# Performance work log

Hardware: AMD Instinct MI355X
Metric: run time of the kernel (lower is better)

The kernel has to match this reference:

```python
import jax, jax.numpy as jnp
import numpy as np

H = 100          # hidden_size
D = 2 * H        # mod / q_enc feature dim (BiDAF hidden)
B, L, G, Q = 16, 2048, 12, 64
NEG = -1e30


def _bidaf(c, q, c_mask, q_mask, cw, qw, cqw, bias):
    """BiDAF attention. c:(B,Lc,D) q:(B,Q,D) -> (B,Lc,4D). Eval mode (no dropout)."""
    s0 = c @ cw                                    # (B,Lc,1)
    s1 = jnp.swapaxes(q @ qw, 1, 2)                # (B,1,Q)
    s2 = jnp.einsum('bld,bqd->blq', c * cqw, q)    # (B,Lc,Q)
    s = s0 + s1 + s2 + bias
    p_q = jax.nn.softmax(jnp.where(q_mask[:, None, :] > 0, s, NEG), axis=2)  # c2q
    p_c = jax.nn.softmax(jnp.where(c_mask[:, :, None] > 0, s, NEG), axis=1)  # q2c
    a = p_q @ q                                    # (B,Lc,D)
    qc = jnp.einsum('blq,bld->bqd', p_c, c)        # s2^T @ c, reassociated
    b2 = p_q @ qc                                  # == (p_q @ p_c^T) @ c
    return jnp.concatenate([c, a, c * a, c * b2], axis=-1)


def setup_inputs() -> dict:
    ks = jax.random.split(jax.random.key(0), 16)
    f32 = jnp.float32
    inp = {
        'att': jax.random.normal(ks[0], (B, L, 8 * H), f32),
        'mod': jax.random.normal(ks[1], (B, L, D), f32),
        'gap_indices': jax.random.randint(ks[2], (B, G), 0, L),
        'mask': jnp.ones((B, L), jnp.int32),
        'q_enc': jax.random.normal(ks[3], (B, Q, D), f32),
        'q_mask': jnp.ones((B, Q), jnp.int32),
        'c_weight': jax.random.normal(ks[4], (D, 1), f32) * 0.07,
        'q_weight': jax.random.normal(ks[5], (D, 1), f32) * 0.07,
        'cq_weight': jax.random.normal(ks[6], (1, 1, D), f32) * 0.07,
        'bidaf_bias': jnp.zeros((1,), f32),
        'w_att': jax.random.normal(ks[7], (3 * 8 * H, 1), f32) * 0.02,
        'b_att': jnp.zeros((1,), f32),
        'w_mod': jax.random.normal(ks[8], (3 * 2 * H, 1), f32) * 0.04,
        'b_mod': jnp.zeros((1,), f32),
        'w_att2': jax.random.normal(ks[9], (3 * 8 * H, 1), f32) * 0.02,
        'b_att2': jnp.zeros((1,), f32),
        'w_att_s': jax.random.normal(ks[10], (3 * 8 * H, 1), f32) * 0.02,
        'b_att_s': jnp.zeros((1,), f32),
        'w_mod_s': jax.random.normal(ks[11], (3 * 2 * H, 1), f32) * 0.04,
        'b_mod_s': jnp.zeros((1,), f32),
        'w_att_s2': jax.random.normal(ks[12], (3 * 8 * H, 1), f32) * 0.02,
        'b_att_s2': jnp.zeros((1,), f32),
    }
    return inp


def reference(att, mod, gap_indices, mask, q_enc, q_mask,
              c_weight, q_weight, cq_weight, bidaf_bias,
              w_att, b_att, w_mod, b_mod, w_att2, b_att2,
              w_att_s, b_att_s, w_mod_s, b_mod_s, w_att_s2, b_att_s2):
    Bz, Lz, _ = mod.shape
    idx_b = jnp.arange(Bz)[:, None]
    att_gaps = att[idx_b, gap_indices]            # (B,G,8H)
    mod_gaps = mod[idx_b, gap_indices]            # (B,G,2H)
    att2_gaps = _bidaf(mod_gaps, q_enc, jnp.ones_like(gap_indices), q_mask,
                       c_weight, q_weight, cq_weight, bidaf_bias)  # (B,G,8H)

    maskf = mask.astype(jnp.float32)
    cnt0 = maskf.sum(1)[:, None]                  # (B,1)
    pool0_mod = jnp.concatenate([mod.max(1), mod.sum(1) / cnt0], -1)   # (B,4H)
    pool0_att = jnp.concatenate([att.max(1), att.sum(1) / cnt0], -1)   # (B,16H)
    pool0_att2 = jnp.zeros((Bz, 2 * 8 * H), mod.dtype)                 # (B,1600)

    positions = jnp.arange(Lz)[None, :]           # (1,L)

    def step(carry, gid):                          # gid: (B,)
        wm = (positions >= gid[:, None] - 12) & (positions <= gid[:, None] + 12) & (mask > 0)
        wmf = wm.astype(jnp.float32)
        cnt = wmf.sum(1)[:, None]                  # (B,1)
        modw = mod * wmf[:, :, None]
        attw = att * wmf[:, :, None]
        pm = jnp.concatenate([modw.max(1), modw.sum(1) / cnt], -1)
        pa = jnp.concatenate([attw.max(1), attw.sum(1) / cnt], -1)
        a2 = _bidaf(modw, q_enc, wm.astype(jnp.int32), q_mask,
                    c_weight, q_weight, cq_weight, bidaf_bias)   # (B,L,8H)
        p2 = jnp.concatenate([a2.max(1), a2.sum(1) / cnt], -1)
        return carry, (pm, pa, p2)

    _, (pm, pa, p2) = jax.lax.scan(step, None, gap_indices[:, 1:].T)
    pools_mod = jnp.concatenate([pool0_mod[:, None], jnp.swapaxes(pm, 0, 1)], 1)   # (B,G,4H)
    pools_att = jnp.concatenate([pool0_att[:, None], jnp.swapaxes(pa, 0, 1)], 1)   # (B,G,16H)
    pools_att2 = jnp.concatenate([pool0_att2[:, None], jnp.swapaxes(p2, 0, 1)], 1) # (B,G,16H)

    mod_cat = jnp.concatenate([mod_gaps, pools_mod], -1)      # (B,G,6H)
    att_cat = jnp.concatenate([att_gaps, pools_att], -1)      # (B,G,24H)
    att2_cat = jnp.concatenate([att2_gaps, pools_att2], -1)   # (B,G,24H)

    logit_start = (att_cat[:, :1] @ w_att_s + b_att_s
                   + mod_cat[:, :1] @ w_mod_s + b_mod_s
                   + att2_cat[:, :1] @ w_att_s2 + b_att_s2)
    logit_rest = (att_cat[:, 1:] @ w_att + b_att
                  + mod_cat[:, 1:] @ w_mod + b_mod
                  + att2_cat[:, 1:] @ w_att2 + b_att2)
    logits = jnp.concatenate([logit_start, logit_rest], 1)[:, :, 0]   # (B,G)
    return logits
```

## Files before the change

kernel.cpp:

```cpp
#include <hip/hip_runtime.h>
#include <math.h>


constexpr int LL = 2048;
constexpr int GG = 12;
constexpr int QQ = 64;
constexpr int DD = 200;
constexpr int AD = 800;
constexpr int NW = 25;
constexpr float FNEG = -1e30f;

constexpr size_t OFF_QET  = 0;
constexpr size_t OFF_S1   = 204800;
constexpr size_t OFF_PART = 205824;
constexpr size_t OFF_PAM  = 205840;
constexpr size_t OFF_PAS  = 410640;
constexpr size_t OFF_PMM  = 615440;
constexpr size_t OFF_PMS  = 666640;

__device__ __forceinline__ float dot4(const float4 a, const float4 b) {
  return a.x*b.x + a.y*b.y + a.z*b.z + a.w*b.w;
}
__device__ __forceinline__ float4 max4(const float4 a, const float4 b) {
  return make_float4(fmaxf(a.x,b.x), fmaxf(a.y,b.y), fmaxf(a.z,b.z), fmaxf(a.w,b.w));
}
__device__ __forceinline__ float4 add4(const float4 a, const float4 b) {
  return make_float4(a.x+b.x, a.y+b.y, a.z+b.z, a.w+b.w);
}
__device__ __forceinline__ float wave_sum(float v) {
  #pragma unroll
  for (int o = 32; o > 0; o >>= 1) v += __shfl_down(v, o, 64);
  return v;
}

__global__ __launch_bounds__(256) void k_pre(const float* __restrict__ q_enc,
                                             const float* __restrict__ qwv,
                                             const float* __restrict__ cqw,
                                             float* __restrict__ ws) {
  const int qs = blockIdx.x, b = blockIdx.y, t = threadIdx.x;
  const int ql = t >> 4, jt = t & 15;
  const int q = qs * 16 + ql;
  float s1 = 0.f;
  #pragma unroll
  for (int k = 0; k < 4; ++k) {
    const int j = jt + 16 * k;
    if (j < 50) {
      const float4 v  = ((const float4*)(q_enc + ((size_t)b * QQ + q) * DD))[j];
      const float4 cw = ((const float4*)cqw)[j];
      const float4 qw = ((const float4*)qwv)[j];
      float4 o; o.x = v.x*cw.x; o.y = v.y*cw.y; o.z = v.z*cw.z; o.w = v.w*cw.w;
      ((float4*)(ws + OFF_QET + (size_t)b * 12800))[j * 64 + q] = o;
      s1 += dot4(v, qw);
    }
  }
  s1 += __shfl_xor(s1, 1, 64);
  s1 += __shfl_xor(s1, 2, 64);
  s1 += __shfl_xor(s1, 4, 64);
  s1 += __shfl_xor(s1, 8, 64);
  if (jt == 0) ws[OFF_S1 + b * QQ + q] = s1;
}

__global__ __launch_bounds__(1024) void k_pool_att(const float* __restrict__ att,
                                                   float* __restrict__ ws) {
  const int ch = blockIdx.x, b = blockIdx.y, t = threadIdx.x;
  __shared__ __align__(16) float stA[4][200][8];
  if (t < 800) {
    const int qt = t / 200, col = t - qt * 200;
    const float4* p = (const float4*)(att + ((size_t)b * LL + ch * 128 + qt * 32) * AD) + col;
    float4 m = make_float4(-3e38f, -3e38f, -3e38f, -3e38f);
    float4 s = make_float4(0.f, 0.f, 0.f, 0.f);
    for (int i = 0; i < 32; i += 4) {
      const float4 v0 = p[(size_t)(i + 0) * 200];
      const float4 v1 = p[(size_t)(i + 1) * 200];
      const float4 v2 = p[(size_t)(i + 2) * 200];
      const float4 v3 = p[(size_t)(i + 3) * 200];
      m = max4(m, max4(max4(v0, v1), max4(v2, v3)));
      s = add4(s, add4(add4(v0, v1), add4(v2, v3)));
    }
    *(float4*)&stA[qt][col][0] = m;
    *(float4*)&stA[qt][col][4] = s;
  }
  __syncthreads();
  if (t < 200) {
    float4 m = *(const float4*)&stA[0][t][0];
    float4 s = *(const float4*)&stA[0][t][4];
    #pragma unroll
    for (int qt = 1; qt < 4; ++qt) {
      m = max4(m, *(const float4*)&stA[qt][t][0]);
      s = add4(s, *(const float4*)&stA[qt][t][4]);
    }
    ((float4*)(ws + OFF_PAM))[(size_t)(b * 16 + ch) * 200 + t] = m;
    ((float4*)(ws + OFF_PAS))[(size_t)(b * 16 + ch) * 200 + t] = s;
  }
}

__global__ __launch_bounds__(512) void k_pool_mod(const float* __restrict__ mod,
                                                  float* __restrict__ ws) {
  const int ch = blockIdx.x, b = blockIdx.y, t = threadIdx.x;
  __shared__ __align__(16) float stM[8][50][8];
  if (t < 400) {
    const int rg = t / 50, col = t - rg * 50;
    const float4* p = (const float4*)(mod + ((size_t)b * LL + ch * 128 + rg * 16) * DD) + col;
    float4 m = make_float4(-3e38f, -3e38f, -3e38f, -3e38f);
    float4 s = make_float4(0.f, 0.f, 0.f, 0.f);
    for (int i = 0; i < 16; i += 4) {
      const float4 v0 = p[(size_t)(i + 0) * 50];
      const float4 v1 = p[(size_t)(i + 1) * 50];
      const float4 v2 = p[(size_t)(i + 2) * 50];
      const float4 v3 = p[(size_t)(i + 3) * 50];
      m = max4(m, max4(max4(v0, v1), max4(v2, v3)));
      s = add4(s, add4(add4(v0, v1), add4(v2, v3)));
    }
    *(float4*)&stM[rg][col][0] = m;
    *(float4*)&stM[rg][col][4] = s;
  }
  __syncthreads();
  if (t < 50) {
    float4 m = *(const float4*)&stM[0][t][0];
    float4 s = *(const float4*)&stM[0][t][4];
    #pragma unroll
    for (int rg = 1; rg < 8; ++rg) {
      m = max4(m, *(const float4*)&stM[rg][t][0]);
      s = add4(s, *(const float4*)&stM[rg][t][4]);
    }
    ((float4*)(ws + OFF_PMM))[(size_t)(b * 16 + ch) * 50 + t] = m;
    ((float4*)(ws + OFF_PMS))[(size_t)(b * 16 + ch) * 50 + t] = s;
  }
}

__global__ __launch_bounds__(1024, 4) void k_main(
    const float* __restrict__ att, const float* __restrict__ mod,
    const int* __restrict__ gaps, const int* __restrict__ mask,
    const float* __restrict__ q_enc, const int* __restrict__ q_mask,
    const float* __restrict__ cwv,
    const float* __restrict__ wA,  const float* __restrict__ bA,
    const float* __restrict__ wM,  const float* __restrict__ bM,
    const float* __restrict__ wA2, const float* __restrict__ bA2,
    const float* __restrict__ wAs, const float* __restrict__ wMs,
    const float* __restrict__ wA2s,
    float* __restrict__ ws, float* __restrict__ out) {

  const int x = blockIdx.x, b = blockIdx.y, t = threadIdx.x;
  const int w = t >> 6, lane = t & 63;

  __shared__ __align__(16) float cA[37][200];
  __shared__ __align__(16) float sA[37][68];
  __shared__ __align__(16) float pqS[27][68];
  __shared__ __align__(16) float pqT[64][28];
  __shared__ __align__(16) float MTS[25][28];
  __shared__ float MgS[12];
  __shared__ float statS[4][2600];
  __shared__ float s0A[37];
  __shared__ float s1S[64];
  __shared__ float red[16];
  __shared__ int rowsS[37];
  __shared__ int qmS[64];
  __shared__ int cntS, gidS;

  if (t >= 64 && t < 80) ((int4*)qmS)[t - 64] = ((const int4*)(q_mask + b * QQ))[t - 64];
  if (w == 15) {
    const int gid = gaps[b * GG + x];
    if (lane == 0) gidS = gid;
    if (lane >= 32 && lane < 44) rowsS[NW + lane - 32] = gaps[b * GG + (lane - 32)];
    bool ok = false; int pos = 0;
    if (x > 0 && lane < NW) {
      const int lo = max(gid - 12, 0), hi = min(gid + 12, LL - 1);
      pos = lo + lane;
      ok = (pos <= hi) && (mask[(size_t)b * LL + pos] > 0);
    }
    const unsigned long long bal = __ballot(ok);
    if (lane < NW) rowsS[lane] = gid;
    if (ok) rowsS[__popcll(bal & ((1ull << lane) - 1ull))] = pos;
    if (lane == 0) cntS = (x > 0) ? (int)__popcll(bal) : 0;
  }
  __syncthreads();

  for (int i = t; i < 37 * 50; i += 1024) {
    const int rr = i / 50, dc = (i - rr * 50) * 4;
    *(float4*)&cA[rr][dc] = *(const float4*)(mod + ((size_t)b * LL + rowsS[rr]) * DD + dc);
  }
  if (t >= 896 && t < 960) s1S[t - 896] = ws[OFF_S1 + b * QQ + (t - 896)];
  __syncthreads();

  if (t < 37) {
    float a = 0.f;
    for (int k = 0; k < 50; ++k)
      a += dot4(*(const float4*)&cA[t][k * 4], ((const float4*)cwv)[k]);
    s0A[t] = a;
  }
  {
    const int rBase = (x == 0) ? NW : 0;
    const int nR = (x == 0) ? GG : 37;
    const float* qet = ws + OFF_QET + (size_t)b * 12800;
    const int r0 = w, r1 = w + 16, r2r = w + 32;
    const bool h0 = r0 < nR, h1 = r1 < nR, h2 = r2r < nR;
    const int rr0 = rBase + (h0 ? r0 : 0);
    const int rr1 = rBase + (h1 ? r1 : 0);
    const int rr2 = rBase + (h2 ? r2r : 0);
    float a0 = 0.f, a1 = 0.f, a2 = 0.f;
    for (int j = 0; j < 50; ++j) {
      const float4 qv = ((const float4*)qet)[j * 64 + lane];
      a0 += dot4(*(const float4*)&cA[rr0][j * 4], qv);
      a1 += dot4(*(const float4*)&cA[rr1][j * 4], qv);
      a2 += dot4(*(const float4*)&cA[rr2][j * 4], qv);
    }
    if (h0) sA[rr0][lane] = a0;
    if (h1) sA[rr1][lane] = a1;
    if (h2) sA[rr2][lane] = a2;
  }
  __syncthreads();

  float pv[8];
  const bool rowAct = (t < 216);
  const int grp = t >> 3, j8 = t & 7;
  if (rowAct) {
    if (grp < NW && grp >= cntS) {
      #pragma unroll
      for (int k = 0; k < 8; ++k) pv[k] = 0.f;
    } else {
      const int srow = (grp < NW) ? grp : (NW + x);
      #pragma unroll
      for (int k = 0; k < 8; ++k) {
        const int q = j8 * 8 + k;
        const float s = (grp == 26) ? s1S[q] : (sA[srow][q] + s1S[q]);
        pv[k] = (qmS[q] > 0) ? s : FNEG;
      }
      float m = pv[0];
      #pragma unroll
      for (int k = 1; k < 8; ++k) m = fmaxf(m, pv[k]);
      m = fmaxf(m, __shfl_xor(m, 1, 64));
      m = fmaxf(m, __shfl_xor(m, 2, 64));
      m = fmaxf(m, __shfl_xor(m, 4, 64));
      float sum = 0.f;
      #pragma unroll
      for (int k = 0; k < 8; ++k) { pv[k] = expf(pv[k] - m); sum += pv[k]; }
      sum += __shfl_xor(sum, 1, 64);
      sum += __shfl_xor(sum, 2, 64);
      sum += __shfl_xor(sum, 4, 64);
      const float inv = 1.f / sum;
      #pragma unroll
      for (int k = 0; k < 8; ++k) pv[k] *= inv;
    }
  }
  float pcv[37];
  const bool colAct = (t >= 256 && t < 320);
  if (colAct) {
    const int qc = t - 256;
    const int cnt = cntS;
    float mW = -3e38f;
    for (int r = 0; r < NW; ++r)
      if (r < cnt) mW = fmaxf(mW, sA[r][qc] + s0A[r]);
    float sum = 0.f;
    for (int r = 0; r < NW; ++r) {
      float e = 0.f;
      if (r < cnt) { e = expf(sA[r][qc] + s0A[r] - mW); sum += e; }
      pcv[r] = e;
    }
    const float inv = (cnt > 0) ? (1.f / sum) : 0.f;
    for (int r = 0; r < NW; ++r) pcv[r] *= inv;
    float mG = -3e38f;
    for (int g = 0; g < GG; ++g) mG = fmaxf(mG, sA[NW + g][qc] + s0A[NW + g]);
    sum = 0.f;
    for (int g = 0; g < GG; ++g) {
      const float e = expf(sA[NW + g][qc] + s0A[NW + g] - mG);
      pcv[NW + g] = e; sum += e;
    }
    const float invg = 1.f / sum;
    for (int g = 0; g < GG; ++g) pcv[NW + g] *= invg;
  }
  __syncthreads();

  if (rowAct) {
    *(float4*)&pqS[grp][j8 * 8]     = make_float4(pv[0], pv[1], pv[2], pv[3]);
    *(float4*)&pqS[grp][j8 * 8 + 4] = make_float4(pv[4], pv[5], pv[6], pv[7]);
    #pragma unroll
    for (int k = 0; k < 8; ++k) pqT[j8 * 8 + k][grp] = pv[k];
  }
  if (colAct) {
    const int qc = t - 256;
    for (int r = 0; r < 37; ++r) sA[r][qc] = pcv[r];
  }
  if (t >= 320 && t < 384) pqT[t - 320][27] = 0.f;
  __syncthreads();

  if (t < 637) {
    int pr, pc;
    if (t < 625) { pr = t / 25; pc = t - pr * 25; }
    else         { pr = 25;     pc = NW + (t - 625); }
    float s = 0.f;
    #pragma unroll 4
    for (int k4 = 0; k4 < 16; ++k4)
      s += dot4(*(const float4*)&pqS[pr][k4 * 4], *(const float4*)&sA[pc][k4 * 4]);
    if (t < 625) MTS[pc][pr] = s; else MgS[t - 625] = s;
  }
  if (t >= 640 && t < 715) { const int e = t - 640; MTS[e / 3][25 + e % 3] = 0.f; }
  __syncthreads();

  {
    const int slab = t >> 8, d = t & 255;
    if (d < 200) {
      const int r0 = 8 * slab;
      float a[8] = {0,0,0,0,0,0,0,0};
      float bb[8] = {0,0,0,0,0,0,0,0};
      const float* qe = q_enc + (size_t)b * QQ * DD + d;
      if (slab < 3) {
        #pragma unroll 4
        for (int q = 0; q < QQ; ++q) {
          const float vq = qe[(size_t)q * DD];
          const float4 p0 = *(const float4*)&pqT[q][r0];
          const float4 p1 = *(const float4*)&pqT[q][r0 + 4];
          a[0] += p0.x*vq; a[1] += p0.y*vq; a[2] += p0.z*vq; a[3] += p0.w*vq;
          a[4] += p1.x*vq; a[5] += p1.y*vq; a[6] += p1.z*vq; a[7] += p1.w*vq;
        }
        #pragma unroll 5
        for (int r2 = 0; r2 < NW; ++r2) {
          const float cv = cA[r2][d];
          const float4 m0 = *(const float4*)&MTS[r2][r0];
          const float4 m1 = *(const float4*)&MTS[r2][r0 + 4];
          bb[0] += m0.x*cv; bb[1] += m0.y*cv; bb[2] += m0.z*cv; bb[3] += m0.w*cv;
          bb[4] += m1.x*cv; bb[5] += m1.y*cv; bb[6] += m1.z*cv; bb[7] += m1.w*cv;
        }
      } else {
        #pragma unroll 4
        for (int q = 0; q < QQ; ++q) {
          const float vq = qe[(size_t)q * DD];
          const float4 p0 = *(const float4*)&pqT[q][24];
          a[0] += p0.x*vq; a[1] += p0.y*vq; a[2] += p0.z*vq; a[3] += p0.w*vq;
        }
        #pragma unroll 5
        for (int r2 = 0; r2 < NW; ++r2) {
          const float cv = cA[r2][d];
          const float4 m0 = *(const float4*)&MTS[r2][24];
          bb[0] += m0.x*cv;
        }
      }
      const int cnt = cntS;
      float mxa = -3e38f, sma = 0.f, mxca = -3e38f, smca = 0.f;
      float mxcb = -3e38f, smcb = 0.f, aG = 0.f;
      if (slab < 3) {
        #pragma unroll
        for (int k = 0; k < 8; ++k) {
          const int r = r0 + k;
          if (r < cnt) {
            const float av = a[k], cv = cA[r][d];
            mxa = fmaxf(mxa, av); sma += av;
            const float ca = cv * av; mxca = fmaxf(mxca, ca); smca += ca;
            const float cb = cv * bb[k]; mxcb = fmaxf(mxcb, cb); smcb += cb;
          }
        }
      } else {
        if (24 < cnt) {
          const float av = a[0], cv = cA[24][d];
          mxa = fmaxf(mxa, av); sma += av;
          const float ca = cv * av; mxca = fmaxf(mxca, ca); smca += ca;
          const float cb = cv * bb[0]; mxcb = fmaxf(mxcb, cb); smcb += cb;
        }
        aG = a[1];
        const float ac = a[2];
        mxa = fmaxf(mxa, ac);
        sma += (float)(LL - cnt) * ac;
      }
      float* sp = &statS[slab][d * 13];
      sp[0] = mxa; sp[1] = sma; sp[2] = mxca; sp[3] = smca;
      sp[4] = mxcb; sp[5] = smcb; sp[6] = aG;
    }
  }
  __syncthreads();

  float acc = 0.f;
  const float* wa  = x ? wA  : wAs;
  const float* wm  = x ? wM  : wMs;
  const float* wa2 = x ? wA2 : wA2s;
  if (t < 200) {
    const int d = t;
    float mxa = -3e38f, sma = 0.f, mxca = 0.f, smca = 0.f, mxcb = 0.f, smcb = 0.f;
    #pragma unroll
    for (int s = 0; s < 4; ++s) {
      const float* sp = &statS[s][d * 13];
      mxa = fmaxf(mxa, sp[0]); sma += sp[1];
      mxca = fmaxf(mxca, sp[2]); smca += sp[3];
      mxcb = fmaxf(mxcb, sp[4]); smcb += sp[5];
    }
    const float aG = statS[3][d * 13 + 6];
    const float cg = cA[NW + x][d];
    float b2G = 0.f;
    #pragma unroll
    for (int g = 0; g < GG; ++g) b2G += MgS[g] * cA[NW + g][d];
    acc += cg * (wa2[d] + wm[d]) + aG * wa2[DD + d]
         + cg * aG * wa2[2 * DD + d] + cg * b2G * wa2[3 * DD + d];
    if (x > 0) {
      const int cnt = cntS;
      const float invc = 1.f / (float)cnt;
      float mxc = 0.f, smc = 0.f;
      #pragma unroll
      for (int r = 0; r < NW; ++r) {
        if (r < cnt) { const float cv = cA[r][d]; mxc = fmaxf(mxc, cv); smc += cv; }
      }
      acc += mxc * (wm[DD + d] + wa2[AD + d]) + smc * invc * (wm[2 * DD + d] + wa2[2 * AD + d]);
      acc += mxa * wa2[AD + DD + d]       + sma  * invc * wa2[2 * AD + DD + d];
      acc += mxca * wa2[AD + 2 * DD + d]  + smca * invc * wa2[2 * AD + 2 * DD + d];
      acc += mxcb * wa2[AD + 3 * DD + d]  + smcb * invc * wa2[2 * AD + 3 * DD + d];
    }
    const float4 w0 = ((const float4*)wa)[t];
    const float4 ar = ((const float4*)(att + ((size_t)b * LL + gidS) * AD))[t];
    acc += dot4(ar, w0);
    if (x > 0) {
      const float4 w1 = ((const float4*)(wa + AD))[t];
      const float4 w2 = ((const float4*)(wa + 2 * AD))[t];
      float4 mx = make_float4(0.f, 0.f, 0.f, 0.f);
      float4 sm = make_float4(0.f, 0.f, 0.f, 0.f);
      const int cnt = cntS;
      for (int r = 0; r < NW; ++r) {
        if (r < cnt) {
          const float4 v = ((const float4*)(att + ((size_t)b * LL + rowsS[r]) * AD))[t];
          mx = max4(mx, v); sm = add4(sm, v);
        }
      }
      const float invc = 1.f / (float)cnt;
      acc += dot4(mx, w1) + invc * dot4(sm, w2);
    }
  }
  const float wsum = wave_sum(acc);
  if (lane == 0) red[w] = wsum;
  __syncthreads();
  if (t == 0) {
    float s = 0.f;
    #pragma unroll
    for (int i = 0; i < 16; ++i) s += red[i];
    if (x == 0) ws[OFF_PART + b] = s;
    else out[b * GG + x] = s + bA[0] + bM[0] + bA2[0];
  }
}

__global__ __launch_bounds__(256) void k_finish(const int* __restrict__ mask,
    const float* __restrict__ wAs, const float* __restrict__ bAs,
    const float* __restrict__ wMs, const float* __restrict__ bMs,
    const float* __restrict__ bA2s,
    const float* __restrict__ ws, float* __restrict__ out) {
  const int b = blockIdx.x, t = threadIdx.x;
  __shared__ float red[4];
  __shared__ float inv0S;
  int cm = 0;
  for (int l = t; l < LL; l += 256) cm += (mask[(size_t)b * LL + l] > 0) ? 1 : 0;
  const float cf = wave_sum((float)cm);
  if ((t & 63) == 0) red[t >> 6] = cf;
  __syncthreads();
  if (t == 0) inv0S = 1.f / (red[0] + red[1] + red[2] + red[3]);
  __syncthreads();
  const float inv0 = inv0S;
  float acc = 0.f;
  if (t < 200) {
    float4 m = ((const float4*)(ws + OFF_PAM))[(size_t)(b * 16) * 200 + t];
    float4 s = ((const float4*)(ws + OFF_PAS))[(size_t)(b * 16) * 200 + t];
    for (int ch = 1; ch < 16; ++ch) {
      m = max4(m, ((const float4*)(ws + OFF_PAM))[(size_t)(b * 16 + ch) * 200 + t]);
      s = add4(s, ((const float4*)(ws + OFF_PAS))[(size_t)(b * 16 + ch) * 200 + t]);
    }
    acc += dot4(m, ((const float4*)(wAs + AD))[t]) + inv0 * dot4(s, ((const float4*)(wAs + 2 * AD))[t]);
  }
  if (t < 50) {
    float4 m = ((const float4*)(ws + OFF_PMM))[(size_t)(b * 16) * 50 + t];
    float4 s = ((const float4*)(ws + OFF_PMS))[(size_t)(b * 16) * 50 + t];
    for (int ch = 1; ch < 16; ++ch) {
      m = max4(m, ((const float4*)(ws + OFF_PMM))[(size_t)(b * 16 + ch) * 50 + t]);
      s = add4(s, ((const float4*)(ws + OFF_PMS))[(size_t)(b * 16 + ch) * 50 + t]);
    }
    acc += dot4(m, ((const float4*)(wMs + DD))[t]) + inv0 * dot4(s, ((const float4*)(wMs + 2 * DD))[t]);
  }
  __syncthreads();
  const float tot = wave_sum(acc);
  if ((t & 63) == 0) red[t >> 6] = tot;
  __syncthreads();
  if (t == 0)
    out[b * GG] = red[0] + red[1] + red[2] + red[3] + ws[OFF_PART + b]
                + bAs[0] + bMs[0] + bA2s[0];
}

extern "C" void kernel_launch(void* const* d_in, const int* in_sizes, int n_in,
                              void* d_out, int out_size, void* d_ws, size_t ws_size,
                              hipStream_t stream) {
  (void)in_sizes; (void)n_in; (void)out_size; (void)ws_size;
  const float* att    = (const float*)d_in[0];
  const float* mod    = (const float*)d_in[1];
  const int*   gaps   = (const int*)  d_in[2];
  const int*   mask   = (const int*)  d_in[3];
  const float* q_enc  = (const float*)d_in[4];
  const int*   q_mask = (const int*)  d_in[5];
  const float* cwv    = (const float*)d_in[6];
  const float* qwv    = (const float*)d_in[7];
  const float* cqw    = (const float*)d_in[8];
  const float* wA     = (const float*)d_in[10];
  const float* bA     = (const float*)d_in[11];
  const float* wM     = (const float*)d_in[12];
  const float* bM     = (const float*)d_in[13];
  const float* wA2    = (const float*)d_in[14];
  const float* bA2    = (const float*)d_in[15];
  const float* wAs    = (const float*)d_in[16];
  const float* bAs    = (const float*)d_in[17];
  const float* wMs    = (const float*)d_in[18];
  const float* bMs    = (const float*)d_in[19];
  const float* wA2s   = (const float*)d_in[20];
  const float* bA2s   = (const float*)d_in[21];
  float* out = (float*)d_out;
  float* ws  = (float*)d_ws;

  hipLaunchKernelGGL(k_pre, dim3(4, 16), dim3(256), 0, stream, q_enc, qwv, cqw, ws);
  hipLaunchKernelGGL(k_main, dim3(GG, 16), dim3(1024), 0, stream,
                     att, mod, gaps, mask, q_enc, q_mask, cwv,
                     wA, bA, wM, bM, wA2, bA2, wAs, wMs, wA2s, ws, out);
  hipLaunchKernelGGL(k_pool_att, dim3(16, 16), dim3(1024), 0, stream, att, ws);
  hipLaunchKernelGGL(k_pool_mod, dim3(16, 16), dim3(512), 0, stream, mod, ws);
  hipLaunchKernelGGL(k_finish, dim3(16), dim3(256), 0, stream,
                     mask, wAs, bAs, wMs, bMs, bA2s, ws, out);
}
```

Before: 266.8 us.

## Merge BiDAF main and pooling kernels into one heterogeneous launch with 512-thread blocks

Combines the per-gap BiDAF kernel and the two full-sequence pooling kernels into one launch. Block IDs below 192 run the attention work, and the remaining blocks run the att and mod max/sum pooling. Block size drops from 1024 to 512 threads, with more rows per wave, and the two-slab work split is rebalanced. Pool chunking changes to 32 att chunks and 4 mod chunks per batch, and shared memory is unioned to cut LDS per block. The aim is to remove two launches and let the small BiDAF grid overlap with the bandwidth-bound pooling, at the cost of more per-thread registers and longer dependence chains.

New measurement: 249.5 us. 1.07x faster.

```diff
diff --git a/kernel.cpp b/kernel.cpp
--- a/kernel.cpp
+++ b/kernel.cpp
@@ -14,9 +14,9 @@
 constexpr size_t OFF_S1   = 204800;
 constexpr size_t OFF_PART = 205824;
 constexpr size_t OFF_PAM  = 205840;
-constexpr size_t OFF_PAS  = 410640;
-constexpr size_t OFF_PMM  = 615440;
-constexpr size_t OFF_PMS  = 666640;
+constexpr size_t OFF_PAS  = OFF_PAM + 16 * 32 * 800;
+constexpr size_t OFF_PMM  = OFF_PAS + 16 * 32 * 800;
+constexpr size_t OFF_PMS  = OFF_PMM + 16 * 4 * 200;
 
 __device__ __forceinline__ float dot4(const float4 a, const float4 b) {
   return a.x*b.x + a.y*b.y + a.z*b.z + a.w*b.w;
@@ -32,6 +32,23 @@
   for (int o = 32; o > 0; o >>= 1) v += __shfl_down(v, o, 64);
   return v;
 }
+
+struct BidafLDS {
+  float cA[37][200];
+  float sA[37][68];
+  float pqS[27][68];
+  float pqT[64][28];
+  float MTS[25][28];
+  float statS[2][1408];
+  float MgS[12];
+  float s0A[40];
+  float s1S[64];
+  float red[8];
+  int   rowsS[40];
+  int   qmS[64];
+  int   cntS, gidS;
+};
+struct PoolLDS { float st[3208]; };
 
 __global__ __launch_bounds__(256) void k_pre(const float* __restrict__ q_enc,
                                              const float* __restrict__ qwv,
@@ -60,75 +77,7 @@
   if (jt == 0) ws[OFF_S1 + b * QQ + q] = s1;
 }
 
-__global__ __launch_bounds__(1024) void k_pool_att(const float* __restrict__ att,
-                                                   float* __restrict__ ws) {
-  const int ch = blockIdx.x, b = blockIdx.y, t = threadIdx.x;
-  __shared__ __align__(16) float stA[4][200][8];
-  if (t < 800) {
-    const int qt = t / 200, col = t - qt * 200;
-    const float4* p = (const float4*)(att + ((size_t)b * LL + ch * 128 + qt * 32) * AD) + col;
-    float4 m = make_float4(-3e38f, -3e38f, -3e38f, -3e38f);
-    float4 s = make_float4(0.f, 0.f, 0.f, 0.f);
-    for (int i = 0; i < 32; i += 4) {
-      const float4 v0 = p[(size_t)(i + 0) * 200];
-      const float4 v1 = p[(size_t)(i + 1) * 200];
-      const float4 v2 = p[(size_t)(i + 2) * 200];
-      const float4 v3 = p[(size_t)(i + 3) * 200];
-      m = max4(m, max4(max4(v0, v1), max4(v2, v3)));
-      s = add4(s, add4(add4(v0, v1), add4(v2, v3)));
-    }
-    *(float4*)&stA[qt][col][0] = m;
-    *(float4*)&stA[qt][col][4] = s;
-  }
-  __syncthreads();
-  if (t < 200) {
-    float4 m = *(const float4*)&stA[0][t][0];
-    float4 s = *(const float4*)&stA[0][t][4];
-    #pragma unroll
-    for (int qt = 1; qt < 4; ++qt) {
-      m = max4(m, *(const float4*)&stA[qt][t][0]);
-      s = add4(s, *(const float4*)&stA[qt][t][4]);
-    }
-    ((float4*)(ws + OFF_PAM))[(size_t)(b * 16 + ch) * 200 + t] = m;
-    ((float4*)(ws + OFF_PAS))[(size_t)(b * 16 + ch) * 200 + t] = s;
-  }
-}
-
-__global__ __launch_bounds__(512) void k_pool_mod(const float* __restrict__ mod,
-                                                  float* __restrict__ ws) {
-  const int ch = blockIdx.x, b = blockIdx.y, t = threadIdx.x;
-  __shared__ __align__(16) float stM[8][50][8];
-  if (t < 400) {
-    const int rg = t / 50, col = t - rg * 50;
-    const float4* p = (const float4*)(mod + ((size_t)b * LL + ch * 128 + rg * 16) * DD) + col;
-    float4 m = make_float4(-3e38f, -3e38f, -3e38f, -3e38f);
-    float4 s = make_float4(0.f, 0.f, 0.f, 0.f);
-    for (int i = 0; i < 16; i += 4) {
-      const float4 v0 = p[(size_t)(i + 0) * 50];
-      const float4 v1 = p[(size_t)(i + 1) * 50];
-      const float4 v2 = p[(size_t)(i + 2) * 50];
-      const float4 v3 = p[(size_t)(i + 3) * 50];
-      m = max4(m, max4(max4(v0, v1), max4(v2, v3)));
-      s = add4(s, add4(add4(v0, v1), add4(v2, v3)));
-    }
-    *(float4*)&stM[rg][col][0] = m;
-    *(float4*)&stM[rg][col][4] = s;
-  }
-  __syncthreads();
-  if (t < 50) {
-    float4 m = *(const float4*)&stM[0][t][0];
-    float4 s = *(const float4*)&stM[0][t][4];
-    #pragma unroll
-    for (int rg = 1; rg < 8; ++rg) {
-      m = max4(m, *(const float4*)&stM[rg][t][0]);
-      s = add4(s, *(const float4*)&stM[rg][t][4]);
-    }
-    ((float4*)(ws + OFF_PMM))[(size_t)(b * 16 + ch) * 50 + t] = m;
-    ((float4*)(ws + OFF_PMS))[(size_t)(b * 16 + ch) * 50 + t] = s;
-  }
-}
-
-__global__ __launch_bounds__(1024, 4) void k_main(
+__global__ __launch_bounds__(512, 4) void k_uni(
     const float* __restrict__ att, const float* __restrict__ mod,
     const int* __restrict__ gaps, const int* __restrict__ mask,
     const float* __restrict__ q_enc, const int* __restrict__ q_mask,
@@ -140,28 +89,81 @@
     const float* __restrict__ wA2s,
     float* __restrict__ ws, float* __restrict__ out) {
 
-  const int x = blockIdx.x, b = blockIdx.y, t = threadIdx.x;
+  __shared__ __align__(16) unsigned char LDSU[sizeof(BidafLDS)];
+  const int bid = blockIdx.x, t = threadIdx.x;
+
+  if (bid >= 192) {
+    PoolLDS& P = *reinterpret_cast<PoolLDS*>(LDSU);
+    if (bid < 704) {
+      const int i = bid - 192, b = i >> 5, ch = i & 31;
+      if (t < 400) {
+        const int qt = t / 200, col = t - qt * 200;
+        const float4* p = (const float4*)(att + ((size_t)b * LL + ch * 64 + qt * 32) * AD) + col;
+        float4 m = make_float4(-3e38f, -3e38f, -3e38f, -3e38f);
+        float4 s = make_float4(0.f, 0.f, 0.f, 0.f);
+        for (int r = 0; r < 32; r += 4) {
+          const float4 v0 = p[(size_t)(r + 0) * 200];
+          const float4 v1 = p[(size_t)(r + 1) * 200];
+          const float4 v2 = p[(size_t)(r + 2) * 200];
+          const float4 v3 = p[(size_t)(r + 3) * 200];
+          m = max4(m, max4(max4(v0, v1), max4(v2, v3)));
+          s = add4(s, add4(add4(v0, v1), add4(v2, v3)));
+        }
+        *(float4*)&P.st[(qt * 200 + col) * 8]     = m;
+        *(float4*)&P.st[(qt * 200 + col) * 8 + 4] = s;
+      }
+      __syncthreads();
+      if (t < 200) {
+        float4 m = max4(*(const float4*)&P.st[t * 8],
+                        *(const float4*)&P.st[(200 + t) * 8]);
+        float4 s = add4(*(const float4*)&P.st[t * 8 + 4],
+                        *(const float4*)&P.st[(200 + t) * 8 + 4]);
+        ((float4*)(ws + OFF_PAM))[((size_t)b * 32 + ch) * 200 + t] = m;
+        ((float4*)(ws + OFF_PAS))[((size_t)b * 32 + ch) * 200 + t] = s;
+      }
+    } else {
+      const int i = bid - 704, b = i >> 2, q4 = i & 3;
+      if (t < 400) {
+        const int rg = t / 50, col = t - rg * 50;
+        const float4* p = (const float4*)(mod + ((size_t)b * LL + q4 * 512 + rg * 64) * DD) + col;
+        float4 m = make_float4(-3e38f, -3e38f, -3e38f, -3e38f);
+        float4 s = make_float4(0.f, 0.f, 0.f, 0.f);
+        for (int r = 0; r < 64; r += 4) {
+          const float4 v0 = p[(size_t)(r + 0) * 50];
+          const float4 v1 = p[(size_t)(r + 1) * 50];
+          const float4 v2 = p[(size_t)(r + 2) * 50];
+          const float4 v3 = p[(size_t)(r + 3) * 50];
+          m = max4(m, max4(max4(v0, v1), max4(v2, v3)));
+          s = add4(s, add4(add4(v0, v1), add4(v2, v3)));
+        }
+        *(float4*)&P.st[(rg * 50 + col) * 8]     = m;
+        *(float4*)&P.st[(rg * 50 + col) * 8 + 4] = s;
+      }
+      __syncthreads();
+      if (t < 50) {
+        float4 m = *(const float4*)&P.st[t * 8];
+        float4 s = *(const float4*)&P.st[t * 8 + 4];
+        #pragma unroll
+        for (int rg = 1; rg < 8; ++rg) {
+          m = max4(m, *(const float4*)&P.st[(rg * 50 + t) * 8]);
+          s = add4(s, *(const float4*)&P.st[(rg * 50 + t) * 8 + 4]);
+        }
+        ((float4*)(ws + OFF_PMM))[((size_t)b * 4 + q4) * 50 + t] = m;
+        ((float4*)(ws + OFF_PMS))[((size_t)b * 4 + q4) * 50 + t] = s;
+      }
+    }
+    return;
+  }
+
+  BidafLDS& L = *reinterpret_cast<BidafLDS*>(LDSU);
+  const int b = bid / 12, x = bid - 12 * (bid / 12);
   const int w = t >> 6, lane = t & 63;
 
-  __shared__ __align__(16) float cA[37][200];
-  __shared__ __align__(16) float sA[37][68];
-  __shared__ __align__(16) float pqS[27][68];
-  __shared__ __align__(16) float pqT[64][28];
-  __shared__ __align__(16) float MTS[25][28];
-  __shared__ float MgS[12];
-  __shared__ float statS[4][2600];
-  __shared__ float s0A[37];
-  __shared__ float s1S[64];
-  __shared__ float red[16];
-  __shared__ int rowsS[37];
-  __shared__ int qmS[64];
-  __shared__ int cntS, gidS;
-
-  if (t >= 64 && t < 80) ((int4*)qmS)[t - 64] = ((const int4*)(q_mask + b * QQ))[t - 64];
-  if (w == 15) {
+  if (t >= 64 && t < 80) ((int4*)L.qmS)[t - 64] = ((const int4*)(q_mask + b * QQ))[t - 64];
+  if (w == 7) {
     const int gid = gaps[b * GG + x];
-    if (lane == 0) gidS = gid;
-    if (lane >= 32 && lane < 44) rowsS[NW + lane - 32] = gaps[b * GG + (lane - 32)];
+    if (lane == 0) L.gidS = gid;
+    if (lane >= 32 && lane < 44) L.rowsS[NW + lane - 32] = gaps[b * GG + (lane - 32)];
     bool ok = false; int pos = 0;
     if (x > 0 && lane < NW) {
       const int lo = max(gid - 12, 0), hi = min(gid + 12, LL - 1);
@@ -169,44 +171,50 @@
       ok = (pos <= hi) && (mask[(size_t)b * LL + pos] > 0);
     }
     const unsigned long long bal = __ballot(ok);
-    if (lane < NW) rowsS[lane] = gid;
-    if (ok) rowsS[__popcll(bal & ((1ull << lane) - 1ull))] = pos;
-    if (lane == 0) cntS = (x > 0) ? (int)__popcll(bal) : 0;
-  }
-  __syncthreads();
-
-  for (int i = t; i < 37 * 50; i += 1024) {
-    const int rr = i / 50, dc = (i - rr * 50) * 4;
-    *(float4*)&cA[rr][dc] = *(const float4*)(mod + ((size_t)b * LL + rowsS[rr]) * DD + dc);
-  }
-  if (t >= 896 && t < 960) s1S[t - 896] = ws[OFF_S1 + b * QQ + (t - 896)];
+    if (lane < NW) L.rowsS[lane] = gid;
+    if (ok) L.rowsS[__popcll(bal & ((1ull << lane) - 1ull))] = pos;
+    if (lane == 0) L.cntS = (x > 0) ? (int)__popcll(bal) : 0;
+  }
+  __syncthreads();
+
+  for (int i2 = t; i2 < 37 * 50; i2 += 512) {
+    const int rr = i2 / 50, dc = (i2 - rr * 50) * 4;
+    *(float4*)&L.cA[rr][dc] = *(const float4*)(mod + ((size_t)b * LL + L.rowsS[rr]) * DD + dc);
+  }
+  if (t >= 384 && t < 448) L.s1S[t - 384] = ws[OFF_S1 + b * QQ + (t - 384)];
   __syncthreads();
 
   if (t < 37) {
     float a = 0.f;
     for (int k = 0; k < 50; ++k)
-      a += dot4(*(const float4*)&cA[t][k * 4], ((const float4*)cwv)[k]);
-    s0A[t] = a;
+      a += dot4(*(const float4*)&L.cA[t][k * 4], ((const float4*)cwv)[k]);
+    L.s0A[t] = a;
   }
   {
     const int rBase = (x == 0) ? NW : 0;
     const int nR = (x == 0) ? GG : 37;
     const float* qet = ws + OFF_QET + (size_t)b * 12800;
-    const int r0 = w, r1 = w + 16, r2r = w + 32;
-    const bool h0 = r0 < nR, h1 = r1 < nR, h2 = r2r < nR;
+    const int r0 = w, r1 = w + 8, r2r = w + 16, r3 = w + 24, r4 = w + 32;
+    const bool h0 = r0 < nR, h1 = r1 < nR, h2 = r2r < nR, h3 = r3 < nR, h4 = r4 < nR;
     const int rr0 = rBase + (h0 ? r0 : 0);
     const int rr1 = rBase + (h1 ? r1 : 0);
     const int rr2 = rBase + (h2 ? r2r : 0);
-    float a0 = 0.f, a1 = 0.f, a2 = 0.f;
+    const int rr3 = rBase + (h3 ? r3 : 0);
+    const int rr4 = rBase + (h4 ? r4 : 0);
+    float a0 = 0.f, a1 = 0.f, a2 = 0.f, a3 = 0.f, a4 = 0.f;
     for (int j = 0; j < 50; ++j) {
       const float4 qv = ((const float4*)qet)[j * 64 + lane];
-      a0 += dot4(*(const float4*)&cA[rr0][j * 4], qv);
-      a1 += dot4(*(const float4*)&cA[rr1][j * 4], qv);
-      a2 += dot4(*(const float4*)&cA[rr2][j * 4], qv);
-    }
-    if (h0) sA[rr0][lane] = a0;
-    if (h1) sA[rr1][lane] = a1;
-    if (h2) sA[rr2][lane] = a2;
+      a0 += dot4(*(const float4*)&L.cA[rr0][j * 4], qv);
+      a1 += dot4(*(const float4*)&L.cA[rr1][j * 4], qv);
+      a2 += dot4(*(const float4*)&L.cA[rr2][j * 4], qv);
+      a3 += dot4(*(const float4*)&L.cA[rr3][j * 4], qv);
+      a4 += dot4(*(const float4*)&L.cA[rr4][j * 4], qv);
+    }
+    if (h0) L.sA[rr0][lane] = a0;
+    if (h1) L.sA[rr1][lane] = a1;
+    if (h2) L.sA[rr2][lane] = a2;
+    if (h3) L.sA[rr3][lane] = a3;
+    if (h4) L.sA[rr4][lane] = a4;
   }
   __syncthreads();
 
@@ -214,7 +222,7 @@
   const bool rowAct = (t < 216);
   const int grp = t >> 3, j8 = t & 7;
   if (rowAct) {
-    if (grp < NW && grp >= cntS) {
+    if (grp < NW && grp >= L.cntS) {
       #pragma unroll
       for (int k = 0; k < 8; ++k) pv[k] = 0.f;
     } else {
@@ -222,8 +230,8 @@
       #pragma unroll
       for (int k = 0; k < 8; ++k) {
         const int q = j8 * 8 + k;
-        const float s = (grp == 26) ? s1S[q] : (sA[srow][q] + s1S[q]);
-        pv[k] = (qmS[q] > 0) ? s : FNEG;
+        const float s = (grp == 26) ? L.s1S[q] : (L.sA[srow][q] + L.s1S[q]);
+        pv[k] = (L.qmS[q] > 0) ? s : FNEG;
       }
       float m = pv[0];
       #pragma unroll
@@ -246,23 +254,23 @@
   const bool colAct = (t >= 256 && t < 320);
   if (colAct) {
     const int qc = t - 256;
-    const int cnt = cntS;
-    float mW = -3e38f;
+    const int cnt = L.cntS;
+    float mW = -3.0e38f;
     for (int r = 0; r < NW; ++r)
-      if (r < cnt) mW = fmaxf(mW, sA[r][qc] + s0A[r]);
+      if (r < cnt) mW = fmaxf(mW, L.sA[r][qc] + L.s0A[r]);
     float sum = 0.f;
     for (int r = 0; r < NW; ++r) {
       float e = 0.f;
-      if (r < cnt) { e = expf(sA[r][qc] + s0A[r] - mW); sum += e; }
+      if (r < cnt) { e = expf(L.sA[r][qc] + L.s0A[r] - mW); sum += e; }
       pcv[r] = e;
     }
     const float inv = (cnt > 0) ? (1.f / sum) : 0.f;
     for (int r = 0; r < NW; ++r) pcv[r] *= inv;
-    float mG = -3e38f;
-    for (int g = 0; g < GG; ++g) mG = fmaxf(mG, sA[NW + g][qc] + s0A[NW + g]);
+    float mG = -3.0e38f;
+    for (int g = 0; g < GG; ++g) mG = fmaxf(mG, L.sA[NW + g][qc] + L.s0A[NW + g]);
     sum = 0.f;
     for (int g = 0; g < GG; ++g) {
-      const float e = expf(sA[NW + g][qc] + s0A[NW + g] - mG);
+      const float e = expf(L.sA[NW + g][qc] + L.s0A[NW + g] - mG);
       pcv[NW + g] = e; sum += e;
     }
     const float invg = 1.f / sum;
@@ -271,96 +279,93 @@
   __syncthreads();
 
   if (rowAct) {
-    *(float4*)&pqS[grp][j8 * 8]     = make_float4(pv[0], pv[1], pv[2], pv[3]);
-    *(float4*)&pqS[grp][j8 * 8 + 4] = make_float4(pv[4], pv[5], pv[6], pv[7]);
+    *(float4*)&L.pqS[grp][j8 * 8]     = make_float4(pv[0], pv[1], pv[2], pv[3]);
+    *(float4*)&L.pqS[grp][j8 * 8 + 4] = make_float4(pv[4], pv[5], pv[6], pv[7]);
     #pragma unroll
-    for (int k = 0; k < 8; ++k) pqT[j8 * 8 + k][grp] = pv[k];
+    for (int k = 0; k < 8; ++k) L.pqT[j8 * 8 + k][grp] = pv[k];
   }
   if (colAct) {
     const int qc = t - 256;
-    for (int r = 0; r < 37; ++r) sA[r][qc] = pcv[r];
-  }
-  if (t >= 320 && t < 384) pqT[t - 320][27] = 0.f;
-  __syncthreads();
-
-  if (t < 637) {
+    for (int r = 0; r < 37; ++r) L.sA[r][qc] = pcv[r];
+  }
+  if (t >= 320 && t < 384) L.pqT[t - 320][27] = 0.f;
+  __syncthreads();
+
+  for (int e = t; e < 637; e += 512) {
     int pr, pc;
-    if (t < 625) { pr = t / 25; pc = t - pr * 25; }
-    else         { pr = 25;     pc = NW + (t - 625); }
+    if (e < 625) { pr = e / 25; pc = e - pr * 25; }
+    else         { pr = 25;     pc = NW + (e - 625); }
     float s = 0.f;
     #pragma unroll 4
     for (int k4 = 0; k4 < 16; ++k4)
-      s += dot4(*(const float4*)&pqS[pr][k4 * 4], *(const float4*)&sA[pc][k4 * 4]);
-    if (t < 625) MTS[pc][pr] = s; else MgS[t - 625] = s;
-  }
-  if (t >= 640 && t < 715) { const int e = t - 640; MTS[e / 3][25 + e % 3] = 0.f; }
+      s += dot4(*(const float4*)&L.pqS[pr][k4 * 4], *(const float4*)&L.sA[pc][k4 * 4]);
+    if (e < 625) L.MTS[pc][pr] = s; else L.MgS[e - 625] = s;
+  }
+  if (t < 75) L.MTS[t / 3][25 + t % 3] = 0.f;
   __syncthreads();
 
   {
     const int slab = t >> 8, d = t & 255;
-    if (d < 200) {
-      const int r0 = 8 * slab;
-      float a[8] = {0,0,0,0,0,0,0,0};
-      float bb[8] = {0,0,0,0,0,0,0,0};
+    if (d < DD) {
+      const int c0 = slab ? 12 : 0;
+      float a[16], bb[16];
+      #pragma unroll
+      for (int k = 0; k < 16; ++k) { a[k] = 0.f; bb[k] = 0.f; }
       const float* qe = q_enc + (size_t)b * QQ * DD + d;
-      if (slab < 3) {
-        #pragma unroll 4
-        for (int q = 0; q < QQ; ++q) {
-          const float vq = qe[(size_t)q * DD];
-          const float4 p0 = *(const float4*)&pqT[q][r0];
-          const float4 p1 = *(const float4*)&pqT[q][r0 + 4];
-          a[0] += p0.x*vq; a[1] += p0.y*vq; a[2] += p0.z*vq; a[3] += p0.w*vq;
-          a[4] += p1.x*vq; a[5] += p1.y*vq; a[6] += p1.z*vq; a[7] += p1.w*vq;
-        }
-        #pragma unroll 5
-        for (int r2 = 0; r2 < NW; ++r2) {
-          const float cv = cA[r2][d];
-          const float4 m0 = *(const float4*)&MTS[r2][r0];
-          const float4 m1 = *(const float4*)&MTS[r2][r0 + 4];
-          bb[0] += m0.x*cv; bb[1] += m0.y*cv; bb[2] += m0.z*cv; bb[3] += m0.w*cv;
-          bb[4] += m1.x*cv; bb[5] += m1.y*cv; bb[6] += m1.z*cv; bb[7] += m1.w*cv;
-        }
-      } else {
-        #pragma unroll 4
-        for (int q = 0; q < QQ; ++q) {
-          const float vq = qe[(size_t)q * DD];
-          const float4 p0 = *(const float4*)&pqT[q][24];
-          a[0] += p0.x*vq; a[1] += p0.y*vq; a[2] += p0.z*vq; a[3] += p0.w*vq;
-        }
-        #pragma unroll 5
-        for (int r2 = 0; r2 < NW; ++r2) {
-          const float cv = cA[r2][d];
-          const float4 m0 = *(const float4*)&MTS[r2][24];
-          bb[0] += m0.x*cv;
-        }
-      }
-      const int cnt = cntS;
-      float mxa = -3e38f, sma = 0.f, mxca = -3e38f, smca = 0.f;
-      float mxcb = -3e38f, smcb = 0.f, aG = 0.f;
-      if (slab < 3) {
+      #pragma unroll 4
+      for (int q = 0; q < QQ; ++q) {
+        const float vq = qe[(size_t)q * DD];
+        const float4 p0 = *(const float4*)&L.pqT[q][c0];
+        const float4 p1 = *(const float4*)&L.pqT[q][c0 + 4];
+        const float4 p2 = *(const float4*)&L.pqT[q][c0 + 8];
+        const float4 p3 = *(const float4*)&L.pqT[q][c0 + 12];
+        a[0]+=p0.x*vq; a[1]+=p0.y*vq; a[2]+=p0.z*vq; a[3]+=p0.w*vq;
+        a[4]+=p1.x*vq; a[5]+=p1.y*vq; a[6]+=p1.z*vq; a[7]+=p1.w*vq;
+        a[8]+=p2.x*vq; a[9]+=p2.y*vq; a[10]+=p2.z*vq; a[11]+=p2.w*vq;
+        a[12]+=p3.x*vq; a[13]+=p3.y*vq; a[14]+=p3.z*vq; a[15]+=p3.w*vq;
+      }
+      #pragma unroll 5
+      for (int r2 = 0; r2 < NW; ++r2) {
+        const float cv = L.cA[r2][d];
+        const float4 m0 = *(const float4*)&L.MTS[r2][c0];
+        const float4 m1 = *(const float4*)&L.MTS[r2][c0 + 4];
+        const float4 m2 = *(const float4*)&L.MTS[r2][c0 + 8];
+        const float4 m3 = *(const float4*)&L.MTS[r2][c0 + 12];
+        bb[0]+=m0.x*cv; bb[1]+=m0.y*cv; bb[2]+=m0.z*cv; bb[3]+=m0.w*cv;
+        bb[4]+=m1.x*cv; bb[5]+=m1.y*cv; bb[6]+=m1.z*cv; bb[7]+=m1.w*cv;
+        bb[8]+=m2.x*cv; bb[9]+=m2.y*cv; bb[10]+=m2.z*cv; bb[11]+=m2.w*cv;
+        bb[12]+=m3.x*cv; bb[13]+=m3.y*cv; bb[14]+=m3.z*cv; bb[15]+=m3.w*cv;
+      }
+      const int cnt = L.cntS;
+      float mxa = -3.0e38f, sma = 0.f, mxca = -3.0e38f, smca = 0.f;
+      float mxcb = -3.0e38f, smcb = 0.f, aG = 0.f;
+      if (slab == 0) {
         #pragma unroll
-        for (int k = 0; k < 8; ++k) {
-          const int r = r0 + k;
-          if (r < cnt) {
-            const float av = a[k], cv = cA[r][d];
+        for (int k = 0; k < 13; ++k) {
+          if (k < cnt) {
+            const float av = a[k], cv = L.cA[k][d];
             mxa = fmaxf(mxa, av); sma += av;
             const float ca = cv * av; mxca = fmaxf(mxca, ca); smca += ca;
             const float cb = cv * bb[k]; mxcb = fmaxf(mxcb, cb); smcb += cb;
           }
         }
       } else {
-        if (24 < cnt) {
-          const float av = a[0], cv = cA[24][d];
-          mxa = fmaxf(mxa, av); sma += av;
-          const float ca = cv * av; mxca = fmaxf(mxca, ca); smca += ca;
-          const float cb = cv * bb[0]; mxcb = fmaxf(mxcb, cb); smcb += cb;
+        #pragma unroll
+        for (int k = 1; k < 13; ++k) {
+          const int r = 12 + k;
+          if (r < cnt) {
+            const float av = a[k], cv = L.cA[r][d];
+            mxa = fmaxf(mxa, av); sma += av;
+            const float ca = cv * av; mxca = fmaxf(mxca, ca); smca += ca;
+            const float cb = cv * bb[k]; mxcb = fmaxf(mxcb, cb); smcb += cb;
+          }
         }
-        aG = a[1];
-        const float ac = a[2];
+        aG = a[13];
+        const float ac = a[14];
         mxa = fmaxf(mxa, ac);
         sma += (float)(LL - cnt) * ac;
       }
-      float* sp = &statS[slab][d * 13];
+      float* sp = &L.statS[slab][d * 7];
       sp[0] = mxa; sp[1] = sma; sp[2] = mxca; sp[3] = smca;
       sp[4] = mxcb; sp[5] = smcb; sp[6] = aG;
     }
@@ -371,48 +376,48 @@
   const float* wa  = x ? wA  : wAs;
   const float* wm  = x ? wM  : wMs;
   const float* wa2 = x ? wA2 : wA2s;
-  if (t < 200) {
+  if (t < DD) {
     const int d = t;
-    float mxa = -3e38f, sma = 0.f, mxca = 0.f, smca = 0.f, mxcb = 0.f, smcb = 0.f;
-    #pragma unroll
-    for (int s = 0; s < 4; ++s) {
-      const float* sp = &statS[s][d * 13];
-      mxa = fmaxf(mxa, sp[0]); sma += sp[1];
-      mxca = fmaxf(mxca, sp[2]); smca += sp[3];
-      mxcb = fmaxf(mxcb, sp[4]); smcb += sp[5];
-    }
-    const float aG = statS[3][d * 13 + 6];
-    const float cg = cA[NW + x][d];
+    const float* s0p = &L.statS[0][d * 7];
+    const float* s1p = &L.statS[1][d * 7];
+    const float mxa  = fmaxf(s0p[0], s1p[0]);
+    const float sma  = s0p[1] + s1p[1];
+    const float mxca = fmaxf(0.f, fmaxf(s0p[2], s1p[2]));
+    const float smca = s0p[3] + s1p[3];
+    const float mxcb = fmaxf(0.f, fmaxf(s0p[4], s1p[4]));
+    const float smcb = s0p[5] + s1p[5];
+    const float aG   = s1p[6];
+    const float cg = L.cA[NW + x][d];
     float b2G = 0.f;
     #pragma unroll
-    for (int g = 0; g < GG; ++g) b2G += MgS[g] * cA[NW + g][d];
+    for (int g = 0; g < GG; ++g) b2G += L.MgS[g] * L.cA[NW + g][d];
     acc += cg * (wa2[d] + wm[d]) + aG * wa2[DD + d]
          + cg * aG * wa2[2 * DD + d] + cg * b2G * wa2[3 * DD + d];
     if (x > 0) {
-      const int cnt = cntS;
+      const int cnt = L.cntS;
       const float invc = 1.f / (float)cnt;
       float mxc = 0.f, smc = 0.f;
       #pragma unroll
       for (int r = 0; r < NW; ++r) {
-        if (r < cnt) { const float cv = cA[r][d]; mxc = fmaxf(mxc, cv); smc += cv; }
+        if (r < cnt) { const float cv = L.cA[r][d]; mxc = fmaxf(mxc, cv); smc += cv; }
       }
       acc += mxc * (wm[DD + d] + wa2[AD + d]) + smc * invc * (wm[2 * DD + d] + wa2[2 * AD + d]);
-      acc += mxa * wa2[AD + DD + d]       + sma  * invc * wa2[2 * AD + DD + d];
-      acc += mxca * wa2[AD + 2 * DD + d]  + smca * invc * wa2[2 * AD + 2 * DD + d];
-      acc += mxcb * wa2[AD + 3 * DD + d]  + smcb * invc * wa2[2 * AD + 3 * DD + d];
+      acc += mxa * wa2[AD + DD + d]      + sma  * invc * wa2[2 * AD + DD + d];
+      acc += mxca * wa2[AD + 2 * DD + d] + smca * invc * wa2[2 * AD + 2 * DD + d];
+      acc += mxcb * wa2[AD + 3 * DD + d] + smcb * invc * wa2[2 * AD + 3 * DD + d];
     }
     const float4 w0 = ((const float4*)wa)[t];
-    const float4 ar = ((const float4*)(att + ((size_t)b * LL + gidS) * AD))[t];
+    const float4 ar = ((const float4*)(att + ((size_t)b * LL + L.gidS) * AD))[t];
     acc += dot4(ar, w0);
     if (x > 0) {
       const float4 w1 = ((const float4*)(wa + AD))[t];
       const float4 w2 = ((const float4*)(wa + 2 * AD))[t];
       float4 mx = make_float4(0.f, 0.f, 0.f, 0.f);
       float4 sm = make_float4(0.f, 0.f, 0.f, 0.f);
-      const int cnt = cntS;
+      const int cnt = L.cntS;
       for (int r = 0; r < NW; ++r) {
         if (r < cnt) {
-          const float4 v = ((const float4*)(att + ((size_t)b * LL + rowsS[r]) * AD))[t];
+          const float4 v = ((const float4*)(att + ((size_t)b * LL + L.rowsS[r]) * AD))[t];
           mx = max4(mx, v); sm = add4(sm, v);
         }
       }
@@ -421,12 +426,12 @@
     }
   }
   const float wsum = wave_sum(acc);
-  if (lane == 0) red[w] = wsum;
+  if (lane == 0) L.red[w] = wsum;
   __syncthreads();
   if (t == 0) {
     float s = 0.f;
     #pragma unroll
-    for (int i = 0; i < 16; ++i) s += red[i];
+    for (int i2 = 0; i2 < 8; ++i2) s += L.red[i2];
     if (x == 0) ws[OFF_PART + b] = s;
     else out[b * GG + x] = s + bA[0] + bM[0] + bA2[0];
   }
@@ -450,20 +455,21 @@
   const float inv0 = inv0S;
   float acc = 0.f;
   if (t < 200) {
-    float4 m = ((const float4*)(ws + OFF_PAM))[(size_t)(b * 16) * 200 + t];
-    float4 s = ((const float4*)(ws + OFF_PAS))[(size_t)(b * 16) * 200 + t];
-    for (int ch = 1; ch < 16; ++ch) {
-      m = max4(m, ((const float4*)(ws + OFF_PAM))[(size_t)(b * 16 + ch) * 200 + t]);
-      s = add4(s, ((const float4*)(ws + OFF_PAS))[(size_t)(b * 16 + ch) * 200 + t]);
+    float4 m = ((const float4*)(ws + OFF_PAM))[(size_t)b * 32 * 200 + t];
+    float4 s = ((const float4*)(ws + OFF_PAS))[(size_t)b * 32 * 200 + t];
+    for (int ch = 1; ch < 32; ++ch) {
+      m = max4(m, ((const float4*)(ws + OFF_PAM))[((size_t)b * 32 + ch) * 200 + t]);
+      s = add4(s, ((const float4*)(ws + OFF_PAS))[((size_t)b * 32 + ch) * 200 + t]);
     }
     acc += dot4(m, ((const float4*)(wAs + AD))[t]) + inv0 * dot4(s, ((const float4*)(wAs + 2 * AD))[t]);
   }
   if (t < 50) {
-    float4 m = ((const float4*)(ws + OFF_PMM))[(size_t)(b * 16) * 50 + t];
-    float4 s = ((const float4*)(ws + OFF_PMS))[(size_t)(b * 16) * 50 + t];
-    for (int ch = 1; ch < 16; ++ch) {
-      m = max4(m, ((const float4*)(ws + OFF_PMM))[(size_t)(b * 16 + ch) * 50 + t]);
-      s = add4(s, ((const float4*)(ws + OFF_PMS))[(size_t)(b * 16 + ch) * 50 + t]);
+    float4 m = ((const float4*)(ws + OFF_PMM))[(size_t)b * 4 * 50 + t];
+    float4 s = ((const float4*)(ws + OFF_PMS))[(size_t)b * 4 * 50 + t];
+    #pragma unroll
+    for (int ch = 1; ch < 4; ++ch) {
+      m = max4(m, ((const float4*)(ws + OFF_PMM))[((size_t)b * 4 + ch) * 50 + t]);
+      s = add4(s, ((const float4*)(ws + OFF_PMS))[((size_t)b * 4 + ch) * 50 + t]);
     }
     acc += dot4(m, ((const float4*)(wMs + DD))[t]) + inv0 * dot4(s, ((const float4*)(wMs + 2 * DD))[t]);
   }
@@ -505,11 +511,9 @@
   float* ws  = (float*)d_ws;
 
   hipLaunchKernelGGL(k_pre, dim3(4, 16), dim3(256), 0, stream, q_enc, qwv, cqw, ws);
-  hipLaunchKernelGGL(k_main, dim3(GG, 16), dim3(1024), 0, stream,
+  hipLaunchKernelGGL(k_uni, dim3(768), dim3(512), 0, stream,
                      att, mod, gaps, mask, q_enc, q_mask, cwv,
                      wA, bA, wM, bM, wA2, bA2, wAs, wMs, wA2s, ws, out);
-  hipLaunchKernelGGL(k_pool_att, dim3(16, 16), dim3(1024), 0, stream, att, ws);
-  hipLaunchKernelGGL(k_pool_mod, dim3(16, 16), dim3(512), 0, stream, mod, ws);
   hipLaunchKernelGGL(k_finish, dim3(16), dim3(256), 0, stream,
                      mask, wAs, bAs, wMs, bMs, bA2s, ws, out);
 }
```
